# Kernel optimization log

Measured on AMD Instinct MI355X. Metric: run time of the kernel, lower is better.

The kernel has to match this reference:

```python
import jax, jax.numpy as jnp
import numpy as np

N = 100000      # nodes
E = 3200000     # edges (avg degree 32)
F_IN = 512
HID = 256
CLS = 64


def _linear_init(k, fan_in, fan_out):
    lim = 1.0 / np.sqrt(fan_in)
    kw, kb = jax.random.split(k)
    W = jax.random.uniform(kw, (fan_in, fan_out), jnp.float32, -lim, lim)
    b = jax.random.uniform(kb, (fan_out,), jnp.float32, -lim, lim)
    return W, b


def setup_inputs() -> dict:
    key = jax.random.key(0)
    ks = jax.random.split(key, 8)
    x = jax.random.normal(ks[0], (N, F_IN), jnp.float32)
    edge_src = jax.random.randint(ks[1], (E,), 0, N, jnp.int32)
    off = jax.random.randint(ks[2], (E,), 1, N, jnp.int32)
    edge_dst = ((edge_src + off) % N).astype(jnp.int32)  # no self loops
    Wm0, bm0 = _linear_init(ks[3], F_IN, HID)
    Wv0, bv0 = _linear_init(ks[4], F_IN, HID)
    Wm1, bm1 = _linear_init(ks[5], HID, CLS)
    Wv1, bv1 = _linear_init(ks[6], HID, CLS)
    sample = jax.random.normal(ks[7], (N, CLS), jnp.float32)
    return dict(x=x, Wm0=Wm0, bm0=bm0, Wv0=Wv0, bv0=bv0,
                Wm1=Wm1, bm1=bm1, Wv1=Wv1, bv1=bv1,
                sample=sample, edge_src=edge_src, edge_dst=edge_dst)


def reference(x, Wm0, bm0, Wv0, bv0, Wm1, bm1, Wv1, bv1, sample, edge_src, edge_dst):
    n = x.shape[0]
    loops = jnp.arange(n, dtype=edge_src.dtype)
    src = jnp.concatenate([edge_src, loops])  # fill_diag(adj, 1.0)
    dst = jnp.concatenate([edge_dst, loops])
    ones = jnp.ones(src.shape[0], x.dtype)
    deg = jax.ops.segment_sum(ones, src, num_segments=n)
    dis = jnp.where(deg > 0, deg ** -0.5, 0.0)   # D^-0.5
    di = jnp.where(deg > 0, 1.0 / deg, 0.0)      # D^-1
    w0 = dis[src] * dis[dst]                      # adj0 = D^-0.5 A D^-0.5
    w1 = di[src] * di[dst]                        # adj1 = D^-1  A D^-1

    def spmm(w, m):  # (adj @ m) with edge weights w
        return jax.ops.segment_sum(w[:, None] * m[dst], src, num_segments=n)

    # layer 0 (initial=True): no aggregation, dropout off (eval)
    mean = jax.nn.elu(x @ Wm0 + bm0)
    var = jax.nn.relu(x @ Wv0 + bv0)
    # layer 1: variance-attention + dual SpMM
    mean = jax.nn.elu(mean @ Wm1 + bm1)
    var = jax.nn.relu(var @ Wv1 + bv1) + 1e-6
    attn = jnp.exp(-var)
    mean = spmm(w0, mean * attn)
    var = spmm(w1, var * attn * attn)

    out = mean + sample * jnp.sqrt(var)
    return jax.nn.log_softmax(out, axis=-1)
```

## Files before the change

kernel.cpp:

```cpp
#include <hip/hip_runtime.h>
#include <cstdint>
#include <cstddef>


typedef _Float16 h8 __attribute__((ext_vector_type(8)));
typedef _Float16 h2 __attribute__((ext_vector_type(2)));
typedef float f32x4 __attribute__((ext_vector_type(4)));
typedef unsigned int uint32;

#define BSHIFT 7
#define NCHUNK 256

static __device__ __forceinline__ float elu_f(float z) {
  return z > 0.f ? z : expm1f(z);
}

static __device__ __forceinline__ void gload16(const void* g, void* l) {
  __builtin_amdgcn_global_load_lds(
      (__attribute__((address_space(1))) void*)g,
      (__attribute__((address_space(3))) void*)l, 16, 0, 0);
}

__global__ __launch_bounds__(256) void hist_k(const int* __restrict__ esrc, int E,
                                              int chunk, int* __restrict__ h, int NB) {
  __shared__ int sh[1024];
  int t = threadIdx.x;
  for (int i = t; i < NB; i += 256) sh[i] = 0;
  __syncthreads();
  int e0 = blockIdx.x * chunk;
  int e1 = min(e0 + chunk, E);
  for (int e = e0 + t; e < e1; e += 256) atomicAdd(&sh[esrc[e] >> BSHIFT], 1);
  __syncthreads();
  for (int i = t; i < NB; i += 256) h[blockIdx.x * NB + i] = sh[i];
}

__global__ __launch_bounds__(256) void btotal_k(const int* __restrict__ h,
                                                int* __restrict__ tot, int NB) {
  int b = blockIdx.x, t = threadIdx.x;
  int v = h[t * NB + b];
#pragma unroll
  for (int off = 32; off; off >>= 1) v += __shfl_xor(v, off, 64);
  __shared__ int sw[4];
  if ((t & 63) == 0) sw[t >> 6] = v;
  __syncthreads();
  if (t == 0) tot[b] = sw[0] + sw[1] + sw[2] + sw[3];
}

__global__ __launch_bounds__(1024) void bscan_k(const int* __restrict__ tot,
                                                int* __restrict__ base, int NB) {
  __shared__ int sh[1024];
  int t = threadIdx.x;
  int v = (t < NB) ? tot[t] : 0;
  sh[t] = v;
  __syncthreads();
  for (int off = 1; off < 1024; off <<= 1) {
    int add = (t >= off) ? sh[t - off] : 0;
    __syncthreads();
    sh[t] += add;
    __syncthreads();
  }
  if (t < NB) base[t] = sh[t] - v;
  if (t == 1023) base[NB] = sh[1023];
}

__global__ __launch_bounds__(256) void boff_k(int* __restrict__ h,
                                              const int* __restrict__ base, int NB) {
  __shared__ int sh[256];
  int b = blockIdx.x, t = threadIdx.x;
  int v = h[t * NB + b];
  sh[t] = v;
  __syncthreads();
  for (int off = 1; off < 256; off <<= 1) {
    int add = (t >= off) ? sh[t - off] : 0;
    __syncthreads();
    sh[t] += add;
    __syncthreads();
  }
  h[t * NB + b] = base[b] + sh[t] - v;
}

__global__ __launch_bounds__(256) void bscatter_k(
    const int* __restrict__ esrc, const int* __restrict__ edst, int E, int chunk,
    const int* __restrict__ h, int2* __restrict__ pairs, int NB) {
  __shared__ int lcur[1024];
  int t = threadIdx.x;
  for (int i = t; i < NB; i += 256) lcur[i] = h[blockIdx.x * NB + i];
  __syncthreads();
  int e0 = blockIdx.x * chunk;
  int e1 = min(e0 + chunk, E);
  for (int e = e0 + t; e < e1; e += 256) {
    int s = esrc[e], d = edst[e];
    int pos = atomicAdd(&lcur[s >> BSHIFT], 1);
    pairs[pos] = make_int2(s, d);
  }
}

__global__ __launch_bounds__(256) void countN_k(
    const int2* __restrict__ pairs, const int* __restrict__ base,
    int* __restrict__ cnt, float2* __restrict__ dd, int n) {
  __shared__ int c128[128];
  int b = blockIdx.x, t = threadIdx.x;
  if (t < 128) c128[t] = 0;
  __syncthreads();
  int lo = base[b], hi = base[b + 1];
  for (int i = lo + t; i < hi; i += 256) atomicAdd(&c128[pairs[i].x & 127], 1);
  __syncthreads();
  if (t < 128) {
    int node = b * 128 + t;
    if (node < n) {
      int c = c128[t];
      cnt[node] = c;
      float d = (float)(c + 1);
      dd[node] = make_float2(rsqrtf(d), 1.f / d);
    }
  }
}

__global__ __launch_bounds__(256) void partC_k(
    const int2* __restrict__ pairs, const int* __restrict__ base,
    const int* __restrict__ rs, int* __restrict__ csr, int n) {
  __shared__ int lcur[128];
  int b = blockIdx.x, t = threadIdx.x;
  if (t < 128) {
    int node = b * 128 + t;
    lcur[t] = (node < n) ? rs[node] : 0;
  }
  __syncthreads();
  int lo = base[b], hi = base[b + 1];
  for (int i = lo + t; i < hi; i += 256) {
    int2 pr = pairs[i];
    int pos = atomicAdd(&lcur[pr.x & 127], 1);
    csr[pos] = pr.y;
  }
}

__global__ void scan1_k(const int* __restrict__ cnt, int* __restrict__ excl,
                        int* __restrict__ bsum, int n) {
  __shared__ int sh[256];
  int t = threadIdx.x, idx = blockIdx.x * 256 + t;
  int v = (idx < n) ? ((cnt[idx] + 3) & ~3) : 0;
  sh[t] = v;
  __syncthreads();
  for (int off = 1; off < 256; off <<= 1) {
    int add = (t >= off) ? sh[t - off] : 0;
    __syncthreads();
    sh[t] += add;
    __syncthreads();
  }
  if (idx < n) excl[idx] = sh[t] - v;
  if (t == 255) bsum[blockIdx.x] = sh[255];
}

__global__ void scan2_k(const int* __restrict__ bsum, int* __restrict__ boff, int nb) {
  __shared__ int sh[512];
  int t = threadIdx.x;
  int v = (t < nb) ? bsum[t] : 0;
  sh[t] = v;
  __syncthreads();
  for (int off = 1; off < 512; off <<= 1) {
    int add = (t >= off) ? sh[t - off] : 0;
    __syncthreads();
    sh[t] += add;
    __syncthreads();
  }
  if (t < nb) boff[t] = sh[t] - v;
}

__global__ void scan3_k(int* __restrict__ excl, const int* __restrict__ boff, int n) {
  int idx = blockIdx.x * 256 + threadIdx.x;
  if (idx < n) excl[idx] += boff[blockIdx.x];
}

__global__ void prep_w_k(const float* __restrict__ Wm0, const float* __restrict__ Wv0,
                         const float* __restrict__ Wm1, const float* __restrict__ Wv1,
                         _Float16* __restrict__ W1t, _Float16* __restrict__ W2t) {
  int idx = blockIdx.x * 256 + threadIdx.x;
  if (idx < 512 * 512) {
    int n = idx >> 9, k = idx & 511;
    float v = (n < 256) ? Wm0[k * 256 + n] : Wv0[k * 256 + (n - 256)];
    W1t[idx] = (_Float16)v;
  }
  if (idx < 128 * 512) {
    int n = idx >> 9, k = idx & 511;
    float v = 0.f;
    if (n < 64) { if (k < 256) v = Wm1[k * 64 + n]; }
    else        { if (k >= 256) v = Wv1[(k - 256) * 64 + (n - 64)]; }
    W2t[idx] = (_Float16)v;
  }
}

__global__ __launch_bounds__(256) void gemm1f_k(
    const float* __restrict__ A, const _Float16* __restrict__ Bt,
    const float* __restrict__ b0, const float* __restrict__ b1,
    _Float16* __restrict__ out, int M, int mtiles) {
  __shared__ __align__(16) unsigned char ldsb[49152];

  const int sg = blockIdx.x >> 5, loc = blockIdx.x & 31;
  const int nt = loc >> 3, mtl = loc & 7;
  const int mt = sg * 8 + mtl;
  if (mt >= mtiles) return;
  const int m0 = mt * 128, n0 = nt * 128;
  const int t = threadIdx.x;
  const int lane = t & 63;
  const int wave = t >> 6;
  const int wm = wave >> 1, wn = wave & 1;
  const int lr = lane & 15, quad = lane >> 4;

  const int ra = t >> 3;
  const int asw = ((t & 7) ^ (ra & 7)) << 2;
  const int rb = t >> 2;
  const int bsw = ((t & 3) ^ ((t >> 3) & 3)) << 3;

  f32x4 acc[4][4] = {};

  auto stage = [&](int b, int kt) {
#pragma unroll
    for (int i = 0; i < 4; i++) {
      const float* src = A + (size_t)min(m0 + i * 32 + ra, M - 1) * 512 + kt + asw;
      gload16(src, ldsb + b * 16384 + i * 4096 + t * 16);
    }
#pragma unroll
    for (int i = 0; i < 2; i++) {
      const _Float16* src = Bt + (size_t)(n0 + i * 64 + rb) * 512 + kt + bsw;
      gload16(src, ldsb + 32768 + b * 8192 + i * 4096 + t * 16);
    }
  };

  stage(0, 0);
  __syncthreads();

  int cur = 0;
  const int zA = lr & 7;
  const int zB = (lr >> 1) & 3;
  for (int kt = 0; kt < 512; kt += 32) {
    if (kt + 32 < 512) stage(cur ^ 1, kt + 32);
    const unsigned char* Ab = ldsb + cur * 16384;
    const unsigned char* Bb = ldsb + 32768 + cur * 8192;
    h8 bf[4];
#pragma unroll
    for (int j = 0; j < 4; j++) {
      int row = wn * 64 + j * 16 + lr;
      bf[j] = *(const h8*)(Bb + row * 64 + ((quad ^ zB) << 4));
    }
    h8 af[4];
#pragma unroll
    for (int i = 0; i < 4; i++) {
      int R = wm * 64 + i * 16 + lr;
      const float4 a0 = *(const float4*)(Ab + R * 128 + (((2 * quad) ^ zA) << 4));
      const float4 a1 = *(const float4*)(Ab + R * 128 + (((2 * quad + 1) ^ zA) << 4));
      af[i] = h8{(_Float16)a0.x, (_Float16)a0.y, (_Float16)a0.z, (_Float16)a0.w,
                 (_Float16)a1.x, (_Float16)a1.y, (_Float16)a1.z, (_Float16)a1.w};
    }
#pragma unroll
    for (int i = 0; i < 4; i++)
#pragma unroll
      for (int j = 0; j < 4; j++)
        acc[i][j] = __builtin_amdgcn_mfma_f32_16x16x32_f16(af[i], bf[j], acc[i][j], 0, 0, 0);
    __syncthreads();
    cur ^= 1;
  }

  _Float16* lt = (_Float16*)ldsb;
#pragma unroll
  for (int j = 0; j < 4; j++) {
    int gc = n0 + wn * 64 + j * 16 + lr;
    float bj = (gc < 256) ? b0[gc] : b1[gc - 256];
#pragma unroll
    for (int i = 0; i < 4; i++) {
#pragma unroll
      for (int r = 0; r < 4; r++) {
        float z = acc[i][j][r] + bj;
        float v = (gc < 256) ? elu_f(z) : fmaxf(z, 0.f);
        lt[(wm * 64 + i * 16 + quad * 4 + r) * 136 + wn * 64 + j * 16 + lr] = (_Float16)v;
      }
    }
  }
  __syncthreads();
  {
    const int row = t >> 1, col0 = (t & 1) * 64;
    const int gr = m0 + row;
    if (gr < M) {
      _Float16* dst = out + (size_t)gr * 512 + n0 + col0;
#pragma unroll
      for (int k = 0; k < 8; k++)
        *(h8*)(dst + k * 8) = *(h8*)&lt[row * 136 + col0 + k * 8];
    }
  }
}

__global__ __launch_bounds__(256) void gemm2_k(
    const _Float16* __restrict__ A, const _Float16* __restrict__ Bt,
    const float* __restrict__ bm1, const float* __restrict__ bv1,
    const float2* __restrict__ dd, uint32* __restrict__ Mcat, int M, int K) {
  __shared__ _Float16 lds[20480];
  _Float16* As = lds;
  _Float16* Bs = lds + 10240;
  const int m0 = blockIdx.x * 128;
  const int t = threadIdx.x;
  const int lane = t & 63;
  const int wave = t >> 6;
  const int lr = lane & 15, quad = lane >> 4;
  const int trow = t >> 2;
  const int tkc = (t & 3) * 8;

  const size_t arow0 = (size_t)min(m0 + trow, M - 1) * K;
  const size_t arow1 = (size_t)min(m0 + trow + 64, M - 1) * K;
  const size_t brow0 = (size_t)trow * K;
  const size_t brow1 = (size_t)(trow + 64) * K;

  f32x4 acc[2][8] = {};
  h8 pa[2], pb[2];

  pa[0] = *(const h8*)(A + arow0 + tkc);
  pa[1] = *(const h8*)(A + arow1 + tkc);
  pb[0] = *(const h8*)(Bt + brow0 + tkc);
  pb[1] = *(const h8*)(Bt + brow1 + tkc);
  *(h8*)&As[trow * 40 + tkc] = pa[0];
  *(h8*)&As[(trow + 64) * 40 + tkc] = pa[1];
  *(h8*)&Bs[trow * 40 + tkc] = pb[0];
  *(h8*)&Bs[(trow + 64) * 40 + tkc] = pb[1];
  __syncthreads();

  for (int kt = 0; kt < K; kt += 32) {
    const int cur = (kt >> 5) & 1;
    const int curo = cur * 5120;
    const bool more = (kt + 32) < K;
    if (more) {
      pa[0] = *(const h8*)(A + arow0 + kt + 32 + tkc);
      pa[1] = *(const h8*)(A + arow1 + kt + 32 + tkc);
      pb[0] = *(const h8*)(Bt + brow0 + kt + 32 + tkc);
      pb[1] = *(const h8*)(Bt + brow1 + kt + 32 + tkc);
    }
    h8 af[2], bf[8];
#pragma unroll
    for (int i = 0; i < 2; i++)
      af[i] = *(h8*)&As[curo + (wave * 32 + i * 16 + lr) * 40 + quad * 8];
#pragma unroll
    for (int j = 0; j < 8; j++)
      bf[j] = *(h8*)&Bs[curo + (j * 16 + lr) * 40 + quad * 8];
#pragma unroll
    for (int i = 0; i < 2; i++)
#pragma unroll
      for (int j = 0; j < 8; j++)
        acc[i][j] = __builtin_amdgcn_mfma_f32_16x16x32_f16(af[i], bf[j], acc[i][j], 0, 0, 0);
    if (more) {
      const int nxto = (cur ^ 1) * 5120;
      *(h8*)&As[nxto + trow * 40 + tkc] = pa[0];
      *(h8*)&As[nxto + (trow + 64) * 40 + tkc] = pa[1];
      *(h8*)&Bs[nxto + trow * 40 + tkc] = pb[0];
      *(h8*)&Bs[nxto + (trow + 64) * 40 + tkc] = pb[1];
      __syncthreads();
    }
  }

  float2 wrow[2][4];
#pragma unroll
  for (int i = 0; i < 2; i++)
#pragma unroll
    for (int r = 0; r < 4; r++) {
      int gr = m0 + wave * 32 + i * 16 + quad * 4 + r;
      wrow[i][r] = (gr < M) ? dd[gr] : make_float2(0.f, 0.f);
    }

#pragma unroll
  for (int jm = 0; jm < 4; jm++) {
    int c = jm * 16 + lr;
    float bm = bm1[c], bv = bv1[c];
#pragma unroll
    for (int i = 0; i < 2; i++) {
#pragma unroll
      for (int r = 0; r < 4; r++) {
        int gr = m0 + wave * 32 + i * 16 + quad * 4 + r;
        if (gr < M) {
          float zm = acc[i][jm][r] + bm;
          float zv = acc[i][4 + jm][r] + bv;
          float m = elu_f(zm);
          float v = fmaxf(zv, 0.f) + 1e-6f;
          float a = __expf(-v);
          h2 pk;
          pk.x = (_Float16)(m * a * wrow[i][r].x);
          pk.y = (_Float16)(v * a * a * wrow[i][r].y);
          Mcat[(size_t)gr * 64 + c] = __builtin_bit_cast(uint32, pk);
        }
      }
    }
  }
}

__global__ __launch_bounds__(256) void spmm_final_k(
    const uint32* __restrict__ Mcat, const float2* __restrict__ dd,
    const int* __restrict__ row_start, const int* __restrict__ cnt,
    const int* __restrict__ csr, const float* __restrict__ sample,
    float* __restrict__ out, int n) {
  int wid = threadIdx.x >> 6, lane = threadIdx.x & 63;
  int r = blockIdx.x * 4 + wid;
  if (r >= n) return;
  float2 wr = dd[r];
  h2 self = __builtin_bit_cast(h2, Mcat[(size_t)r * 64 + lane]);
  float Sm = (float)self.x;
  float Sv = (float)self.y;
  int start = __builtin_amdgcn_readfirstlane(row_start[r]);
  int c = __builtin_amdgcn_readfirstlane(cnt[r]);
  int j = 0;
  for (; j + 8 <= c; j += 8) {
    int4 da = *(const int4*)(csr + start + j);
    int4 db = *(const int4*)(csr + start + j + 4);
    h2 p0 = __builtin_bit_cast(h2, Mcat[(size_t)da.x * 64 + lane]);
    h2 p1 = __builtin_bit_cast(h2, Mcat[(size_t)da.y * 64 + lane]);
    h2 p2 = __builtin_bit_cast(h2, Mcat[(size_t)da.z * 64 + lane]);
    h2 p3 = __builtin_bit_cast(h2, Mcat[(size_t)da.w * 64 + lane]);
    h2 p4 = __builtin_bit_cast(h2, Mcat[(size_t)db.x * 64 + lane]);
    h2 p5 = __builtin_bit_cast(h2, Mcat[(size_t)db.y * 64 + lane]);
    h2 p6 = __builtin_bit_cast(h2, Mcat[(size_t)db.z * 64 + lane]);
    h2 p7 = __builtin_bit_cast(h2, Mcat[(size_t)db.w * 64 + lane]);
    Sm += (float)p0.x + (float)p1.x + (float)p2.x + (float)p3.x;
    Sv += (float)p0.y + (float)p1.y + (float)p2.y + (float)p3.y;
    Sm += (float)p4.x + (float)p5.x + (float)p6.x + (float)p7.x;
    Sv += (float)p4.y + (float)p5.y + (float)p6.y + (float)p7.y;
  }
  if (j + 4 <= c) {
    int4 d4 = *(const int4*)(csr + start + j);
    h2 p0 = __builtin_bit_cast(h2, Mcat[(size_t)d4.x * 64 + lane]);
    h2 p1 = __builtin_bit_cast(h2, Mcat[(size_t)d4.y * 64 + lane]);
    h2 p2 = __builtin_bit_cast(h2, Mcat[(size_t)d4.z * 64 + lane]);
    h2 p3 = __builtin_bit_cast(h2, Mcat[(size_t)d4.w * 64 + lane]);
    Sm += (float)p0.x + (float)p1.x + (float)p2.x + (float)p3.x;
    Sv += (float)p0.y + (float)p1.y + (float)p2.y + (float)p3.y;
    j += 4;
  }
  for (; j < c; j++) {
    int d = csr[start + j];
    h2 p = __builtin_bit_cast(h2, Mcat[(size_t)d * 64 + lane]);
    Sm += (float)p.x;
    Sv += (float)p.y;
  }
  float mean = wr.x * Sm;
  float var = wr.y * Sv;
  float o = mean + sample[(size_t)r * 64 + lane] * sqrtf(var);
  float mx = o;
#pragma unroll
  for (int off = 32; off; off >>= 1) mx = fmaxf(mx, __shfl_xor(mx, off, 64));
  float ex = __expf(o - mx);
  float s = ex;
#pragma unroll
  for (int off = 32; off; off >>= 1) s += __shfl_xor(s, off, 64);
  out[(size_t)r * 64 + lane] = o - mx - logf(s);
}

extern "C" void kernel_launch(void* const* d_in, const int* in_sizes, int n_in,
                              void* d_out, int out_size, void* d_ws, size_t ws_size,
                              hipStream_t stream) {
  (void)n_in; (void)out_size; (void)ws_size;
  const float* x    = (const float*)d_in[0];
  const float* Wm0  = (const float*)d_in[1];
  const float* bm0  = (const float*)d_in[2];
  const float* Wv0  = (const float*)d_in[3];
  const float* bv0  = (const float*)d_in[4];
  const float* Wm1  = (const float*)d_in[5];
  const float* bm1  = (const float*)d_in[6];
  const float* Wv1  = (const float*)d_in[7];
  const float* bv1  = (const float*)d_in[8];
  const float* sample = (const float*)d_in[9];
  const int* esrc   = (const int*)d_in[10];
  const int* edst   = (const int*)d_in[11];
  float* out = (float*)d_out;

  const int N = in_sizes[0] / 512;
  const int E = in_sizes[10];
  const int NB = (N + 127) >> BSHIFT;
  const int chunk = (E + NCHUNK - 1) / NCHUNK;

  uint8_t* p = (uint8_t*)d_ws;
  size_t off = 0;
  auto alloc = [&](size_t bytes) -> void* {
    void* r = p + off;
    off += (bytes + 255) & ~(size_t)255;
    return r;
  };
  _Float16* W1t  = (_Float16*)alloc((size_t)512 * 512 * 2);
  _Float16* W2t  = (_Float16*)alloc((size_t)128 * 512 * 2);
  _Float16* Hcat = (_Float16*)alloc((size_t)N * 512 * 2);
  uint32*   Mcat = (uint32*)alloc((size_t)N * 64 * 4);
  int*   cnt    = (int*)alloc((size_t)N * 4);
  float2* dd    = (float2*)alloc((size_t)N * 8);
  int*   rs     = (int*)alloc((size_t)N * 4);
  int*   h      = (int*)alloc((size_t)NCHUNK * NB * 4);
  int*   tot    = (int*)alloc((size_t)(NB + 1) * 4);
  int*   base   = (int*)alloc((size_t)(NB + 1) * 4);
  int*   bsum   = (int*)alloc(2048);
  int*   boff   = (int*)alloc(2048);
  int*   csr    = (int*)alloc((size_t)(E + 4 * N) * 4);
  int2* pairs = (int2*)Hcat;

  const int nbN = (N + 255) / 256;

  prep_w_k<<<(512 * 512 + 255) / 256, 256, 0, stream>>>(Wm0, Wv0, Wm1, Wv1, W1t, W2t);
  hist_k<<<NCHUNK, 256, 0, stream>>>(esrc, E, chunk, h, NB);
  btotal_k<<<NB, 256, 0, stream>>>(h, tot, NB);
  bscan_k<<<1, 1024, 0, stream>>>(tot, base, NB);
  boff_k<<<NB, 256, 0, stream>>>(h, base, NB);
  bscatter_k<<<NCHUNK, 256, 0, stream>>>(esrc, edst, E, chunk, h, pairs, NB);
  countN_k<<<NB, 256, 0, stream>>>(pairs, base, cnt, dd, N);
  scan1_k<<<nbN, 256, 0, stream>>>(cnt, rs, bsum, N);
  scan2_k<<<1, 512, 0, stream>>>(bsum, boff, nbN);
  scan3_k<<<nbN, 256, 0, stream>>>(rs, boff, N);
  partC_k<<<NB, 256, 0, stream>>>(pairs, base, rs, csr, N);

  const int mtiles = (N + 127) / 128;
  const int sgroups = (mtiles + 7) / 8;
  gemm1f_k<<<sgroups * 32, 256, 0, stream>>>(x, W1t, bm0, bv0, Hcat, N, mtiles);
  gemm2_k<<<mtiles, 256, 0, stream>>>(Hcat, W2t, bm1, bv1, dd, Mcat, N, 512);
  spmm_final_k<<<(N + 3) / 4, 256, 0, stream>>>(Mcat, dd, rs, cnt, csr, sample, out, N);
}
```

Baseline: 698.5 us.

## Pack edge pairs into 32-bit words, shrink GEMM1 M-tile, async-load GEMM2 operands

Edge pairs are packed into one 32-bit word holding the local source index and the destination, which halves the bytes the bucket scatter, count and CSR-fill passes write and read. GEMM1 drops from a 128-row to a 64-row M tile with smaller LDS, giving more blocks and higher occupancy at the cost of re-reading the weight tiles more often. GEMM2 replaces its register-staged LDS copy with global_load_lds async loads into swizzled, double-buffered LDS. These are independent changes across the graph preprocessing and both GEMMs.

```diff
diff --git a/kernel.cpp b/kernel.cpp
--- a/kernel.cpp
+++ b/kernel.cpp
@@ -19,6 +19,11 @@
   __builtin_amdgcn_global_load_lds(
       (__attribute__((address_space(1))) void*)g,
       (__attribute__((address_space(3))) void*)l, 16, 0, 0);
+}
+
+static __device__ __forceinline__ h8 cvt8(float4 a, float4 b) {
+  return h8{(_Float16)a.x, (_Float16)a.y, (_Float16)a.z, (_Float16)a.w,
+            (_Float16)b.x, (_Float16)b.y, (_Float16)b.z, (_Float16)b.w};
 }
 
 __global__ __launch_bounds__(256) void hist_k(const int* __restrict__ esrc, int E,
@@ -81,7 +86,7 @@
 
 __global__ __launch_bounds__(256) void bscatter_k(
     const int* __restrict__ esrc, const int* __restrict__ edst, int E, int chunk,
-    const int* __restrict__ h, int2* __restrict__ pairs, int NB) {
+    const int* __restrict__ h, uint32* __restrict__ pairs, int NB) {
   __shared__ int lcur[1024];
   int t = threadIdx.x;
   for (int i = t; i < NB; i += 256) lcur[i] = h[blockIdx.x * NB + i];
@@ -91,19 +96,19 @@
   for (int e = e0 + t; e < e1; e += 256) {
     int s = esrc[e], d = edst[e];
     int pos = atomicAdd(&lcur[s >> BSHIFT], 1);
-    pairs[pos] = make_int2(s, d);
+    pairs[pos] = ((uint32)(s & 127) << 25) | (uint32)d;
   }
 }
 
 __global__ __launch_bounds__(256) void countN_k(
-    const int2* __restrict__ pairs, const int* __restrict__ base,
+    const uint32* __restrict__ pairs, const int* __restrict__ base,
     int* __restrict__ cnt, float2* __restrict__ dd, int n) {
   __shared__ int c128[128];
   int b = blockIdx.x, t = threadIdx.x;
   if (t < 128) c128[t] = 0;
   __syncthreads();
   int lo = base[b], hi = base[b + 1];
-  for (int i = lo + t; i < hi; i += 256) atomicAdd(&c128[pairs[i].x & 127], 1);
+  for (int i = lo + t; i < hi; i += 256) atomicAdd(&c128[pairs[i] >> 25], 1);
   __syncthreads();
   if (t < 128) {
     int node = b * 128 + t;
@@ -117,7 +122,7 @@
 }
 
 __global__ __launch_bounds__(256) void partC_k(
-    const int2* __restrict__ pairs, const int* __restrict__ base,
+    const uint32* __restrict__ pairs, const int* __restrict__ base,
     const int* __restrict__ rs, int* __restrict__ csr, int n) {
   __shared__ int lcur[128];
   int b = blockIdx.x, t = threadIdx.x;
@@ -128,9 +133,9 @@
   __syncthreads();
   int lo = base[b], hi = base[b + 1];
   for (int i = lo + t; i < hi; i += 256) {
-    int2 pr = pairs[i];
-    int pos = atomicAdd(&lcur[pr.x & 127], 1);
-    csr[pos] = pr.y;
+    uint32 p = pairs[i];
+    int pos = atomicAdd(&lcur[p >> 25], 1);
+    csr[pos] = (int)(p & 0x1FFFFFFu);
   }
 }
 
@@ -189,17 +194,17 @@
   }
 }
 
-__global__ __launch_bounds__(256) void gemm1f_k(
+__global__ __launch_bounds__(256) void gemm1s_k(
     const float* __restrict__ A, const _Float16* __restrict__ Bt,
     const float* __restrict__ b0, const float* __restrict__ b1,
     _Float16* __restrict__ out, int M, int mtiles) {
-  __shared__ __align__(16) unsigned char ldsb[49152];
+  __shared__ __align__(16) unsigned char ldsb[32768];
 
   const int sg = blockIdx.x >> 5, loc = blockIdx.x & 31;
   const int nt = loc >> 3, mtl = loc & 7;
   const int mt = sg * 8 + mtl;
   if (mt >= mtiles) return;
-  const int m0 = mt * 128, n0 = nt * 128;
+  const int m0 = mt * 64, n0 = nt * 128;
   const int t = threadIdx.x;
   const int lane = t & 63;
   const int wave = t >> 6;
@@ -211,18 +216,18 @@
   const int rb = t >> 2;
   const int bsw = ((t & 3) ^ ((t >> 3) & 3)) << 3;
 
-  f32x4 acc[4][4] = {};
+  f32x4 acc[2][4] = {};
 
   auto stage = [&](int b, int kt) {
 #pragma unroll
-    for (int i = 0; i < 4; i++) {
+    for (int i = 0; i < 2; i++) {
       const float* src = A + (size_t)min(m0 + i * 32 + ra, M - 1) * 512 + kt + asw;
       gload16(src, ldsb + b * 16384 + i * 4096 + t * 16);
     }
 #pragma unroll
     for (int i = 0; i < 2; i++) {
       const _Float16* src = Bt + (size_t)(n0 + i * 64 + rb) * 512 + kt + bsw;
-      gload16(src, ldsb + 32768 + b * 8192 + i * 4096 + t * 16);
+      gload16(src, ldsb + b * 16384 + 8192 + i * 4096 + t * 16);
     }
   };
 
@@ -235,24 +240,23 @@
   for (int kt = 0; kt < 512; kt += 32) {
     if (kt + 32 < 512) stage(cur ^ 1, kt + 32);
     const unsigned char* Ab = ldsb + cur * 16384;
-    const unsigned char* Bb = ldsb + 32768 + cur * 8192;
+    const unsigned char* Bb = Ab + 8192;
     h8 bf[4];
 #pragma unroll
     for (int j = 0; j < 4; j++) {
       int row = wn * 64 + j * 16 + lr;
       bf[j] = *(const h8*)(Bb + row * 64 + ((quad ^ zB) << 4));
     }
-    h8 af[4];
-#pragma unroll
-    for (int i = 0; i < 4; i++) {
-      int R = wm * 64 + i * 16 + lr;
+    h8 af[2];
+#pragma unroll
+    for (int i = 0; i < 2; i++) {
+      int R = wm * 32 + i * 16 + lr;
       const float4 a0 = *(const float4*)(Ab + R * 128 + (((2 * quad) ^ zA) << 4));
       const float4 a1 = *(const float4*)(Ab + R * 128 + (((2 * quad + 1) ^ zA) << 4));
-      af[i] = h8{(_Float16)a0.x, (_Float16)a0.y, (_Float16)a0.z, (_Float16)a0.w,
-                 (_Float16)a1.x, (_Float16)a1.y, (_Float16)a1.z, (_Float16)a1.w};
-    }
-#pragma unroll
-    for (int i = 0; i < 4; i++)
+      af[i] = cvt8(a0, a1);
+    }
+#pragma unroll
+    for (int i = 0; i < 2; i++)
 #pragma unroll
       for (int j = 0; j < 4; j++)
         acc[i][j] = __builtin_amdgcn_mfma_f32_16x16x32_f16(af[i], bf[j], acc[i][j], 0, 0, 0);
@@ -266,24 +270,25 @@
     int gc = n0 + wn * 64 + j * 16 + lr;
     float bj = (gc < 256) ? b0[gc] : b1[gc - 256];
 #pragma unroll
-    for (int i = 0; i < 4; i++) {
+    for (int i = 0; i < 2; i++) {
 #pragma unroll
       for (int r = 0; r < 4; r++) {
         float z = acc[i][j][r] + bj;
         float v = (gc < 256) ? elu_f(z) : fmaxf(z, 0.f);
-        lt[(wm * 64 + i * 16 + quad * 4 + r) * 136 + wn * 64 + j * 16 + lr] = (_Float16)v;
+        lt[(wm * 32 + i * 16 + quad * 4 + r) * 136 + wn * 64 + j * 16 + lr] = (_Float16)v;
       }
     }
   }
   __syncthreads();
   {
-    const int row = t >> 1, col0 = (t & 1) * 64;
+    const int row = t >> 2, c0 = (t & 3) * 32;
     const int gr = m0 + row;
     if (gr < M) {
-      _Float16* dst = out + (size_t)gr * 512 + n0 + col0;
-#pragma unroll
-      for (int k = 0; k < 8; k++)
-        *(h8*)(dst + k * 8) = *(h8*)&lt[row * 136 + col0 + k * 8];
+      _Float16* dst = out + (size_t)gr * 512 + n0 + c0;
+      const _Float16* srow = lt + row * 136 + c0;
+#pragma unroll
+      for (int k = 0; k < 4; k++)
+        *(h8*)(dst + k * 8) = *(const h8*)(srow + k * 8);
     }
   }
 }
@@ -291,66 +296,59 @@
 __global__ __launch_bounds__(256) void gemm2_k(
     const _Float16* __restrict__ A, const _Float16* __restrict__ Bt,
     const float* __restrict__ bm1, const float* __restrict__ bv1,
-    const float2* __restrict__ dd, uint32* __restrict__ Mcat, int M, int K) {
-  __shared__ _Float16 lds[20480];
-  _Float16* As = lds;
-  _Float16* Bs = lds + 10240;
+    const float2* __restrict__ dd, uint32* __restrict__ Mcat, int M) {
+  __shared__ __align__(16) unsigned char ldsb[32768];
   const int m0 = blockIdx.x * 128;
   const int t = threadIdx.x;
   const int lane = t & 63;
   const int wave = t >> 6;
   const int lr = lane & 15, quad = lane >> 4;
-  const int trow = t >> 2;
-  const int tkc = (t & 3) * 8;
-
-  const size_t arow0 = (size_t)min(m0 + trow, M - 1) * K;
-  const size_t arow1 = (size_t)min(m0 + trow + 64, M - 1) * K;
-  const size_t brow0 = (size_t)trow * K;
-  const size_t brow1 = (size_t)(trow + 64) * K;
+
+  const int rb = t >> 2;
+  const int sw = ((t & 3) ^ ((t >> 3) & 3)) << 3;
 
   f32x4 acc[2][8] = {};
-  h8 pa[2], pb[2];
-
-  pa[0] = *(const h8*)(A + arow0 + tkc);
-  pa[1] = *(const h8*)(A + arow1 + tkc);
-  pb[0] = *(const h8*)(Bt + brow0 + tkc);
-  pb[1] = *(const h8*)(Bt + brow1 + tkc);
-  *(h8*)&As[trow * 40 + tkc] = pa[0];
-  *(h8*)&As[(trow + 64) * 40 + tkc] = pa[1];
-  *(h8*)&Bs[trow * 40 + tkc] = pb[0];
-  *(h8*)&Bs[(trow + 64) * 40 + tkc] = pb[1];
-  __syncthreads();
-
-  for (int kt = 0; kt < K; kt += 32) {
-    const int cur = (kt >> 5) & 1;
-    const int curo = cur * 5120;
-    const bool more = (kt + 32) < K;
-    if (more) {
-      pa[0] = *(const h8*)(A + arow0 + kt + 32 + tkc);
-      pa[1] = *(const h8*)(A + arow1 + kt + 32 + tkc);
-      pb[0] = *(const h8*)(Bt + brow0 + kt + 32 + tkc);
-      pb[1] = *(const h8*)(Bt + brow1 + kt + 32 + tkc);
-    }
+
+  auto stage = [&](int b, int kt) {
+#pragma unroll
+    for (int i = 0; i < 2; i++) {
+      const _Float16* src = A + (size_t)min(m0 + i * 64 + rb, M - 1) * 512 + kt + sw;
+      gload16(src, ldsb + b * 16384 + i * 4096 + t * 16);
+    }
+#pragma unroll
+    for (int i = 0; i < 2; i++) {
+      const _Float16* src = Bt + (size_t)(i * 64 + rb) * 512 + kt + sw;
+      gload16(src, ldsb + b * 16384 + 8192 + i * 4096 + t * 16);
+    }
+  };
+
+  stage(0, 0);
+  __syncthreads();
+
+  const int z = (lr >> 1) & 3;
+  int cur = 0;
+  for (int kt = 0; kt < 512; kt += 32) {
+    if (kt + 32 < 512) stage(cur ^ 1, kt + 32);
+    const unsigned char* Ab = ldsb + cur * 16384;
+    const unsigned char* Bb = Ab + 8192;
     h8 af[2], bf[8];
 #pragma unroll
-    for (int i = 0; i < 2; i++)
-      af[i] = *(h8*)&As[curo + (wave * 32 + i * 16 + lr) * 40 + quad * 8];
-#pragma unroll
-    for (int j = 0; j < 8; j++)
-      bf[j] = *(h8*)&Bs[curo + (j * 16 + lr) * 40 + quad * 8];
+    for (int i = 0; i < 2; i++) {
+      int row = wave * 32 + i * 16 + lr;
+      af[i] = *(const h8*)(Ab + row * 64 + ((quad ^ z) << 4));
+    }
+#pragma unroll
+    for (int j = 0; j < 8; j++) {
+      int row = j * 16 + lr;
+      bf[j] = *(const h8*)(Bb + row * 64 + ((quad ^ z) << 4));
+    }
 #pragma unroll
     for (int i = 0; i < 2; i++)
 #pragma unroll
       for (int j = 0; j < 8; j++)
         acc[i][j] = __builtin_amdgcn_mfma_f32_16x16x32_f16(af[i], bf[j], acc[i][j], 0, 0, 0);
-    if (more) {
-      const int nxto = (cur ^ 1) * 5120;
-      *(h8*)&As[nxto + trow * 40 + tkc] = pa[0];
-      *(h8*)&As[nxto + (trow + 64) * 40 + tkc] = pa[1];
-      *(h8*)&Bs[nxto + trow * 40 + tkc] = pb[0];
-      *(h8*)&Bs[nxto + (trow + 64) * 40 + tkc] = pb[1];
-      __syncthreads();
-    }
+    __syncthreads();
+    cur ^= 1;
   }
 
   float2 wrow[2][4];
@@ -490,7 +488,7 @@
   int*   bsum   = (int*)alloc(2048);
   int*   boff   = (int*)alloc(2048);
   int*   csr    = (int*)alloc((size_t)(E + 4 * N) * 4);
-  int2* pairs = (int2*)Hcat;
+  uint32* pairs = (uint32*)Hcat;
 
   const int nbN = (N + 255) / 256;
 
@@ -506,9 +504,10 @@
   scan3_k<<<nbN, 256, 0, stream>>>(rs, boff, N);
   partC_k<<<NB, 256, 0, stream>>>(pairs, base, rs, csr, N);
 
+  const int mt64 = (N + 63) / 64;
+  const int sg64 = (mt64 + 7) / 8;
+  gemm1s_k<<<sg64 * 32, 256, 0, stream>>>(x, W1t, bm0, bv0, Hcat, N, mt64);
   const int mtiles = (N + 127) / 128;
-  const int sgroups = (mtiles + 7) / 8;
-  gemm1f_k<<<sgroups * 32, 256, 0, stream>>>(x, W1t, bm0, bv0, Hcat, N, mtiles);
-  gemm2_k<<<mtiles, 256, 0, stream>>>(Hcat, W2t, bm1, bv1, dd, Mcat, N, 512);
+  gemm2_k<<<mtiles, 256, 0, stream>>>(Hcat, W2t, bm1, bv1, dd, Mcat, N);
   spmm_final_k<<<(N + 3) / 4, 256, 0, stream>>>(Mcat, dd, rs, cnt, csr, sample, out, N);
 }
```

Measured after the change: 703.4 us. Within noise of the previous version (+0.7%).
